# Kernel optimization log

Measured on AMD Instinct MI355X. Metric: run time of the kernel, lower is better.

## Reference

```python
import jax, jax.numpy as jnp
import numpy as np


def setup_inputs() -> dict:
    key = jax.random.key(0)
    k1, k2 = jax.random.split(key)
    B, S, D = 8, 4096, 1024
    hidden_states = jax.random.normal(k1, (B, S, D), dtype=jnp.float32)
    boundary_mask = jax.random.uniform(k2, (B, S)) < 0.5
    return {"hidden_states": hidden_states, "boundary_mask": boundary_mask}


def reference(hidden_states, boundary_mask):
    # Per-row boolean-mask gather, then pad each row with zeros to the max
    # selected length across the batch. Equivalent to the torch loop:
    #   compressed[i] = hidden_states[i, boundary_mask[i]]  -> pad/stack.
    B, S, D = hidden_states.shape
    counts = jnp.sum(boundary_mask, axis=1)          # [B] number of kept tokens
    max_len = int(jnp.max(counts))                    # data-dependent output length
    # Stable argsort of ~mask puts True (kept) positions first, preserving order.
    order = jnp.argsort(jnp.logical_not(boundary_mask), axis=1, stable=True)[:, :max_len]  # [B, max_len]
    gathered = jnp.take_along_axis(hidden_states, order[:, :, None], axis=1)  # [B, max_len, D]
    valid = jnp.arange(max_len)[None, :] < counts[:, None]                     # [B, max_len]
    return jnp.where(valid[:, :, None], gathered, jnp.zeros((), hidden_states.dtype))
```

## Files before the change

### kernel.cpp

```cpp
#include <hip/hip_runtime.h>
#include <hip/hip_bf16.h>
#include <stdint.h>

__global__ void __launch_bounds__(64)
compact_index_kernel(const uint32_t* __restrict__ mask_words,
                     int S, int max_len,
                     int* __restrict__ idx, int* __restrict__ counts) {
    const int b    = blockIdx.x;
    const int lane = threadIdx.x;

    uint32_t w0 = mask_words[lane];
    bool weird = (w0 > 1u) && (w0 != 0x3F800000u);
    bool bytemode = (__ballot(weird) != 0ULL);

    const uint8_t* mask_bytes = (const uint8_t*)mask_words;
    const size_t row_base = (size_t)b * (size_t)S;

    int total = 0;
    const int nchunk = S / 64;
    for (int cg = 0; cg < nchunk; cg += 8) {
        uint32_t v[8];
        if (bytemode) {
            #pragma unroll
            for (int k = 0; k < 8; ++k)
                v[k] = (uint32_t)mask_bytes[row_base + (size_t)(cg + k) * 64 + lane];
        } else {
            #pragma unroll
            for (int k = 0; k < 8; ++k)
                v[k] = mask_words[row_base + (size_t)(cg + k) * 64 + lane];
        }
        #pragma unroll
        for (int k = 0; k < 8; ++k) {
            unsigned long long bm = __ballot(v[k] != 0u);
            if (v[k] != 0u) {
                int j = total + (int)__popcll(bm & ((1ULL << lane) - 1ULL));
                idx[b * max_len + j] = (cg + k) * 64 + lane;
            }
            total += (int)__popcll(bm);
        }
    }
    if (lane == 0) counts[b] = total;
}

#define ROWS_PER_BLOCK 4

__global__ void __launch_bounds__(256)
gather_pad_kernel(const float* __restrict__ hs,
                  const int* __restrict__ idx,
                  const int* __restrict__ counts,
                  float* __restrict__ out,
                  int S, int D, int max_len) {
    const int b  = blockIdx.y;
    const int t  = threadIdx.x;
    const int j0 = blockIdx.x * ROWS_PER_BLOCK;
    const int cnt = counts[b];

    #pragma unroll
    for (int r = 0; r < ROWS_PER_BLOCK; ++r) {
        const int j = j0 + r;
        if (j >= max_len) break;
        float4 val = make_float4(0.f, 0.f, 0.f, 0.f);
        if (j < cnt) {
            const int s = idx[b * max_len + j];
            const float4* src =
                (const float4*)(hs + ((size_t)b * S + (size_t)s) * (size_t)D);
            val = src[t];
        }
        float4* dst = (float4*)(out + ((size_t)b * max_len + (size_t)j) * (size_t)D);
        dst[t] = val;
    }
}

extern "C" void kernel_launch(void* const* d_in, const int* in_sizes, int n_in,
                              void* d_out, int out_size, void* d_ws, size_t ws_size,
                              hipStream_t stream) {
    const float*    hs   = (const float*)d_in[0];
    const uint32_t* mask = (const uint32_t*)d_in[1];

    const int B  = 8;
    const int BS = in_sizes[1];
    const int S  = BS / B;
    const int D  = in_sizes[0] / BS;
    const int max_len = out_size / (B * D);

    int* counts = (int*)d_ws;
    int* idx    = (int*)((char*)d_ws + 256);

    compact_index_kernel<<<B, 64, 0, stream>>>(mask, S, max_len, idx, counts);

    dim3 grid((max_len + ROWS_PER_BLOCK - 1) / ROWS_PER_BLOCK, B);
    gather_pad_kernel<<<grid, 256, 0, stream>>>(
        (const float*)hs, idx, counts, (float*)d_out, S, D, max_len);
}
```

Before: 33.83 us.

## Parallelize mask compaction across waves and batch gather loads per block

The compaction kernel now uses 16 waves per batch row, each ballot-counting a slice of chunks, with an LDS prefix over wave totals replacing the serial single-wave scan. The gather kernel loads four indices with one int4 read from a padded-stride index buffer and issues all four row loads before the stores to raise memory-level parallelism. The compaction only handles up to 4 chunks per wave, so it assumes S is at most 4096.

```diff
diff --git a/kernel.cpp b/kernel.cpp
--- a/kernel.cpp
+++ b/kernel.cpp
@@ -2,12 +2,16 @@
 #include <hip/hip_bf16.h>
 #include <stdint.h>
 
-__global__ void __launch_bounds__(64)
+#define WAVES_A 16
+
+__global__ void __launch_bounds__(64 * WAVES_A)
 compact_index_kernel(const uint32_t* __restrict__ mask_words,
-                     int S, int max_len,
+                     int S, int stride,
                      int* __restrict__ idx, int* __restrict__ counts) {
     const int b    = blockIdx.x;
-    const int lane = threadIdx.x;
+    const int t    = threadIdx.x;
+    const int wave = t >> 6;
+    const int lane = t & 63;
 
     uint32_t w0 = mask_words[lane];
     bool weird = (w0 > 1u) && (w0 != 0x3F800000u);
@@ -16,58 +20,93 @@
     const uint8_t* mask_bytes = (const uint8_t*)mask_words;
     const size_t row_base = (size_t)b * (size_t)S;
 
-    int total = 0;
     const int nchunk = S / 64;
-    for (int cg = 0; cg < nchunk; cg += 8) {
-        uint32_t v[8];
-        if (bytemode) {
-            #pragma unroll
-            for (int k = 0; k < 8; ++k)
-                v[k] = (uint32_t)mask_bytes[row_base + (size_t)(cg + k) * 64 + lane];
-        } else {
-            #pragma unroll
-            for (int k = 0; k < 8; ++k)
-                v[k] = mask_words[row_base + (size_t)(cg + k) * 64 + lane];
-        }
+    const int cpw    = nchunk / WAVES_A;
+    const int c0     = wave * cpw;
+
+    uint32_t v[8];
+    if (bytemode) {
         #pragma unroll
-        for (int k = 0; k < 8; ++k) {
-            unsigned long long bm = __ballot(v[k] != 0u);
-            if (v[k] != 0u) {
-                int j = total + (int)__popcll(bm & ((1ULL << lane) - 1ULL));
-                idx[b * max_len + j] = (cg + k) * 64 + lane;
-            }
-            total += (int)__popcll(bm);
+        for (int k = 0; k < 4; ++k)
+            if (k < cpw)
+                v[k] = (uint32_t)mask_bytes[row_base + (size_t)(c0 + k) * 64 + lane];
+    } else {
+        #pragma unroll
+        for (int k = 0; k < 4; ++k)
+            if (k < cpw)
+                v[k] = mask_words[row_base + (size_t)(c0 + k) * 64 + lane];
+    }
+
+    unsigned long long bm[4];
+    int wave_total = 0;
+    #pragma unroll
+    for (int k = 0; k < 4; ++k) {
+        if (k < cpw) {
+            bm[k] = __ballot(v[k] != 0u);
+            wave_total += (int)__popcll(bm[k]);
         }
     }
-    if (lane == 0) counts[b] = total;
+
+    __shared__ int wtot[WAVES_A];
+    if (lane == 0) wtot[wave] = wave_total;
+    __syncthreads();
+
+    int base = 0;
+    for (int w = 0; w < wave; ++w) base += wtot[w];
+
+    #pragma unroll
+    for (int k = 0; k < 4; ++k) {
+        if (k < cpw) {
+            if (v[k] != 0u) {
+                int j = base + (int)__popcll(bm[k] & ((1ULL << lane) - 1ULL));
+                idx[(size_t)b * stride + j] = (c0 + k) * 64 + lane;
+            }
+            base += (int)__popcll(bm[k]);
+        }
+    }
+
+    if (t == 0) {
+        int tot = 0;
+        #pragma unroll
+        for (int w = 0; w < WAVES_A; ++w) tot += wtot[w];
+        counts[b] = tot;
+    }
 }
-
-#define ROWS_PER_BLOCK 4
 
 __global__ void __launch_bounds__(256)
 gather_pad_kernel(const float* __restrict__ hs,
                   const int* __restrict__ idx,
                   const int* __restrict__ counts,
                   float* __restrict__ out,
-                  int S, int D, int max_len) {
-    const int b  = blockIdx.y;
-    const int t  = threadIdx.x;
-    const int j0 = blockIdx.x * ROWS_PER_BLOCK;
+                  int S, int D, int max_len, int stride) {
+    const int b   = blockIdx.y;
+    const int t   = threadIdx.x;
+    const int j0  = blockIdx.x * 4;
     const int cnt = counts[b];
 
+    int4 sidx = *(const int4*)(idx + (size_t)b * stride + j0);
+    const int sj[4] = {sidx.x, sidx.y, sidx.z, sidx.w};
+
+    float4 val[4];
     #pragma unroll
-    for (int r = 0; r < ROWS_PER_BLOCK; ++r) {
+    for (int r = 0; r < 4; ++r) {
+        val[r] = make_float4(0.f, 0.f, 0.f, 0.f);
         const int j = j0 + r;
-        if (j >= max_len) break;
-        float4 val = make_float4(0.f, 0.f, 0.f, 0.f);
         if (j < cnt) {
-            const int s = idx[b * max_len + j];
             const float4* src =
-                (const float4*)(hs + ((size_t)b * S + (size_t)s) * (size_t)D);
-            val = src[t];
+                (const float4*)(hs + ((size_t)b * S + (size_t)sj[r]) * (size_t)D);
+            val[r] = src[t];
         }
-        float4* dst = (float4*)(out + ((size_t)b * max_len + (size_t)j) * (size_t)D);
-        dst[t] = val;
+    }
+
+    #pragma unroll
+    for (int r = 0; r < 4; ++r) {
+        const int j = j0 + r;
+        if (j < max_len) {
+            float4* dst =
+                (float4*)(out + ((size_t)b * max_len + (size_t)j) * (size_t)D);
+            dst[t] = val[r];
+        }
     }
 }
 
@@ -82,13 +121,14 @@
     const int S  = BS / B;
     const int D  = in_sizes[0] / BS;
     const int max_len = out_size / (B * D);
+    const int stride  = (max_len + 3) & ~3;
 
     int* counts = (int*)d_ws;
     int* idx    = (int*)((char*)d_ws + 256);
 
-    compact_index_kernel<<<B, 64, 0, stream>>>(mask, S, max_len, idx, counts);
+    compact_index_kernel<<<B, 64 * WAVES_A, 0, stream>>>(mask, S, stride, idx, counts);
 
-    dim3 grid((max_len + ROWS_PER_BLOCK - 1) / ROWS_PER_BLOCK, B);
+    dim3 grid((max_len + 3) / 4, B);
     gather_pad_kernel<<<grid, 256, 0, stream>>>(
-        (const float*)hs, idx, counts, (float*)d_out, S, D, max_len);
+        hs, idx, counts, (float*)d_out, S, D, max_len, stride);
 }
```

Result: faster. 29.69 us (-12.2%).

## Fuse mask compaction into gather kernel with per-block redundant prefix scan

Applied to the files above, without the earlier changes.

Replaces the two-kernel pipeline (a serial single-wave per-row compaction that writes an index array, then a gather/pad kernel) with one kernel. Each block reloads its row's whole mask, builds 16-bit per-thread masks, runs a block-wide prefix scan, and finds the source positions for its 8 output rows. This removes the slow serial compaction launch and the index round trip through memory, at the cost of every block re-reading and re-scanning the full mask row. Rows per block goes from 4 to 8, and all loads are issued before any stores.

```diff
diff --git a/kernel.cpp b/kernel.cpp
--- a/kernel.cpp
+++ b/kernel.cpp
@@ -2,72 +2,95 @@
 #include <hip/hip_bf16.h>
 #include <stdint.h>
 
-__global__ void __launch_bounds__(64)
-compact_index_kernel(const uint32_t* __restrict__ mask_words,
-                     int S, int max_len,
-                     int* __restrict__ idx, int* __restrict__ counts) {
-    const int b    = blockIdx.x;
-    const int lane = threadIdx.x;
+#define ROWS 8
+
+__global__ void __launch_bounds__(256)
+fused_gather_kernel(const float* __restrict__ hs,
+                    const uint32_t* __restrict__ mask_words,
+                    float* __restrict__ out,
+                    int S, int D, int max_len) {
+    const int b    = blockIdx.y;
+    const int t    = threadIdx.x;
+    const int wave = t >> 6;
+    const int lane = t & 63;
+    const int j0   = blockIdx.x * ROWS;
 
     uint32_t w0 = mask_words[lane];
     bool weird = (w0 > 1u) && (w0 != 0x3F800000u);
-    bool bytemode = (__ballot(weird) != 0ULL);
+    const bool bytemode = (__ballot(weird) != 0ULL);
 
-    const uint8_t* mask_bytes = (const uint8_t*)mask_words;
     const size_t row_base = (size_t)b * (size_t)S;
-
-    int total = 0;
-    const int nchunk = S / 64;
-    for (int cg = 0; cg < nchunk; cg += 8) {
-        uint32_t v[8];
-        if (bytemode) {
+    uint32_t m16 = 0;
+    if (bytemode) {
+        const uint4* bp = (const uint4*)((const uint8_t*)mask_words + row_base) + t;
+        uint4 a = *bp;
+        uint32_t wrds[4] = {a.x, a.y, a.z, a.w};
+        #pragma unroll
+        for (int w = 0; w < 4; ++w)
             #pragma unroll
-            for (int k = 0; k < 8; ++k)
-                v[k] = (uint32_t)mask_bytes[row_base + (size_t)(cg + k) * 64 + lane];
-        } else {
-            #pragma unroll
-            for (int k = 0; k < 8; ++k)
-                v[k] = mask_words[row_base + (size_t)(cg + k) * 64 + lane];
-        }
+            for (int k = 0; k < 4; ++k)
+                m16 |= (uint32_t)(((wrds[w] >> (8 * k)) & 0xffu) != 0u) << (w * 4 + k);
+    } else {
+        const uint4* wp = (const uint4*)(mask_words + row_base) + t * 4;
         #pragma unroll
-        for (int k = 0; k < 8; ++k) {
-            unsigned long long bm = __ballot(v[k] != 0u);
-            if (v[k] != 0u) {
-                int j = total + (int)__popcll(bm & ((1ULL << lane) - 1ULL));
-                idx[b * max_len + j] = (cg + k) * 64 + lane;
-            }
-            total += (int)__popcll(bm);
+        for (int q = 0; q < 4; ++q) {
+            uint4 a = wp[q];
+            m16 |= (uint32_t)(a.x != 0u) << (q * 4 + 0);
+            m16 |= (uint32_t)(a.y != 0u) << (q * 4 + 1);
+            m16 |= (uint32_t)(a.z != 0u) << (q * 4 + 2);
+            m16 |= (uint32_t)(a.w != 0u) << (q * 4 + 3);
         }
     }
-    if (lane == 0) counts[b] = total;
-}
+    const int lc = __popc(m16);
 
-#define ROWS_PER_BLOCK 4
+    int scan = lc;
+    #pragma unroll
+    for (int d = 1; d < 64; d <<= 1) {
+        int n = __shfl_up(scan, d, 64);
+        if (lane >= d) scan += n;
+    }
+    __shared__ int wtot[4];
+    if (lane == 63) wtot[wave] = scan;
+    __syncthreads();
+    int wbase = 0;
+    #pragma unroll
+    for (int w = 0; w < 4; ++w) if (w < wave) wbase += wtot[w];
+    const int cnt = wtot[0] + wtot[1] + wtot[2] + wtot[3];
+    const int pre = wbase + scan - lc;
 
-__global__ void __launch_bounds__(256)
-gather_pad_kernel(const float* __restrict__ hs,
-                  const int* __restrict__ idx,
-                  const int* __restrict__ counts,
-                  float* __restrict__ out,
-                  int S, int D, int max_len) {
-    const int b  = blockIdx.y;
-    const int t  = threadIdx.x;
-    const int j0 = blockIdx.x * ROWS_PER_BLOCK;
-    const int cnt = counts[b];
+    __shared__ int found[ROWS];
+    #pragma unroll
+    for (int r = 0; r < ROWS; ++r) {
+        const int j = j0 + r;
+        if (j < cnt && pre <= j && j < pre + lc) {
+            int rem = j - pre;
+            uint32_t m = m16;
+            for (int k = 0; k < rem; ++k) m &= m - 1;
+            found[r] = t * 16 + __builtin_ctz(m);
+        }
+    }
+    __syncthreads();
 
+    float4 val[ROWS];
     #pragma unroll
-    for (int r = 0; r < ROWS_PER_BLOCK; ++r) {
+    for (int r = 0; r < ROWS; ++r) {
+        val[r] = make_float4(0.f, 0.f, 0.f, 0.f);
         const int j = j0 + r;
-        if (j >= max_len) break;
-        float4 val = make_float4(0.f, 0.f, 0.f, 0.f);
         if (j < cnt) {
-            const int s = idx[b * max_len + j];
+            const int s = found[r];
             const float4* src =
                 (const float4*)(hs + ((size_t)b * S + (size_t)s) * (size_t)D);
-            val = src[t];
+            val[r] = src[t];
         }
-        float4* dst = (float4*)(out + ((size_t)b * max_len + (size_t)j) * (size_t)D);
-        dst[t] = val;
+    }
+    #pragma unroll
+    for (int r = 0; r < ROWS; ++r) {
+        const int j = j0 + r;
+        if (j < max_len) {
+            float4* dst =
+                (float4*)(out + ((size_t)b * max_len + (size_t)j) * (size_t)D);
+            dst[t] = val[r];
+        }
     }
 }
 
@@ -83,12 +106,7 @@
     const int D  = in_sizes[0] / BS;
     const int max_len = out_size / (B * D);
 
-    int* counts = (int*)d_ws;
-    int* idx    = (int*)((char*)d_ws + 256);
-
-    compact_index_kernel<<<B, 64, 0, stream>>>(mask, S, max_len, idx, counts);
-
-    dim3 grid((max_len + ROWS_PER_BLOCK - 1) / ROWS_PER_BLOCK, B);
-    gather_pad_kernel<<<grid, 256, 0, stream>>>(
-        (const float*)hs, idx, counts, (float*)d_out, S, D, max_len);
+    dim3 grid((max_len + ROWS - 1) / ROWS, B);
+    fused_gather_kernel<<<grid, 256, 0, stream>>>(
+        hs, mask, (float*)d_out, S, D, max_len);
 }
```

After: 28.58 us. 1.18x faster.
